# Performance work log

Measured on AMD Instinct MI355X. Metric: run time of the kernel, lower is better.

Reference implementation:

```python
import jax, jax.numpy as jnp
import numpy as np

HEAD_DIM = 64
N_HEADS = 64
N_KV = 8
Q_MULT = N_HEADS // N_KV  # 8
HIDDEN = 2880
SLIDING_WINDOW = 128
BASE = 150000.0
INIT_CTX = 4096
SCALING = 32.0
NTK_ALPHA = 1.0   # beta_slow
NTK_BETA = 32.0   # beta_fast
EPS = 1e-5
SM_SCALE = 1.0 / np.sqrt(HEAD_DIM)


def _cos_sin(num_tokens):
    # YaRN-style NTK rope (scaling_factor > 1 branch)
    freq = BASE ** (jnp.arange(0, HEAD_DIM, 2, dtype=jnp.float32) / HEAD_DIM)
    concentration = 0.1 * np.log(SCALING) + 1.0
    d_half = HEAD_DIM // 2
    low = d_half * np.log(INIT_CTX / (NTK_BETA * 2 * np.pi)) / np.log(BASE)
    high = d_half * np.log(INIT_CTX / (NTK_ALPHA * 2 * np.pi)) / np.log(BASE)
    interpolation = 1.0 / (SCALING * freq)
    extrapolation = 1.0 / freq
    ramp = (jnp.arange(d_half, dtype=jnp.float32) - low) / (high - low)
    mask = 1.0 - jnp.clip(ramp, 0.0, 1.0)
    inv_freq = interpolation * (1.0 - mask) + extrapolation * mask
    t = jnp.arange(num_tokens, dtype=jnp.float32)
    freqs = t[:, None] * inv_freq[None, :]  # [n, d/2]
    return jnp.cos(freqs) * concentration, jnp.sin(freqs) * concentration


def _apply_rotary(x, cos, sin):
    # x: [n, h, d]; cos/sin: [n, d/2]
    cos = cos[:, None, :].astype(x.dtype)
    sin = sin[:, None, :].astype(x.dtype)
    x1, x2 = jnp.split(x, 2, axis=-1)
    return jnp.concatenate((x1 * cos - x2 * sin, x2 * cos + x1 * sin), axis=-1)


def _forward(x, norm_w, qkv_w, out_w, sinks):
    b, s, h = x.shape  # b=1
    n = b * s
    # RMSNorm
    var = jnp.mean(jnp.square(x), axis=-1, keepdims=True)
    t = x * jax.lax.rsqrt(var + EPS) * norm_w
    # QKV projection
    qkv = jnp.einsum('bsh,hf->bsf', t, qkv_w)
    q_dim = N_HEADS * HEAD_DIM
    kv_dim = N_KV * HEAD_DIM
    q = qkv[:, :, :q_dim].reshape(n, N_KV, Q_MULT, HEAD_DIM)
    k = qkv[:, :, q_dim:q_dim + kv_dim].reshape(n, N_KV, HEAD_DIM)
    v = qkv[:, :, q_dim + kv_dim:].reshape(n, N_KV, HEAD_DIM)
    # RoPE
    cos, sin = _cos_sin(n)
    q = _apply_rotary(q.reshape(n, -1, HEAD_DIM), cos, sin).reshape(n, N_KV, Q_MULT, HEAD_DIM)
    k = _apply_rotary(k, cos, sin)
    # sdpa with sliding window + sink logits
    qk = jnp.einsum('qhmd,khd->hmqk', q, k) * SM_SCALE  # [N_KV, Q_MULT, n, n]
    i = jnp.arange(n)[:, None]
    j = jnp.arange(n)[None, :]
    neg_inf = jnp.array(-jnp.inf, dtype=qk.dtype)
    banned = (j > i) | (i - j >= SLIDING_WINDOW)  # causal + sliding window
    qk = jnp.where(banned[None, None, :, :], neg_inf, qk)
    S = jnp.broadcast_to(sinks.reshape(N_KV, Q_MULT, 1, 1), (N_KV, Q_MULT, n, 1))
    logits = jnp.concatenate([qk, S], axis=-1)  # [N_KV, Q_MULT, n, n+1]
    w = jax.nn.softmax(logits, axis=-1)[..., :-1]
    attn = jnp.einsum('hmqk,khd->qhmd', w, v).reshape(n, N_HEADS * HEAD_DIM)
    out = jnp.einsum('qf,fh->qh', attn, out_w)  # [n, hidden]
    return x + out  # broadcasts to [b, s, hidden]


def setup_inputs() -> dict:
    key = jax.random.key(0)
    k1, k2, k3, k4, k5 = jax.random.split(key, 5)
    x = jax.random.normal(k1, (1, 2048, HIDDEN), dtype=jnp.float32)
    norm_w = jax.random.uniform(k2, (HIDDEN,), dtype=jnp.float32, minval=0.5, maxval=1.5)
    qkv_w = jax.random.normal(k3, (HIDDEN, HEAD_DIM * (N_HEADS + 2 * N_KV)), dtype=jnp.float32) * 0.02
    out_w = jax.random.normal(k4, (HEAD_DIM * N_HEADS, HIDDEN), dtype=jnp.float32) * 0.02
    sinks = jax.random.normal(k5, (N_HEADS,), dtype=jnp.float32)
    return {"x": x, "norm_w": norm_w, "qkv_w": qkv_w, "out_w": out_w, "sinks": sinks}


def reference(x, norm_w, qkv_w, out_w, sinks):
    return _forward(x, norm_w, qkv_w, out_w, sinks)
```

## Files before the change

### kernel.cpp

```cpp
#include <hip/hip_runtime.h>
#include <math.h>

typedef unsigned short u16;
typedef unsigned int u32;
typedef short bf4 __attribute__((ext_vector_type(4)));
typedef __bf16 bfv8 __attribute__((ext_vector_type(8)));
typedef float f4 __attribute__((ext_vector_type(4)));

#define SEQ 2048
#define HID 2880
#define KPAD 2944
#define QKVN 5120

static __device__ __forceinline__ u16 f2bf(float x) {
  union { float f; u32 u; } v; v.f = x;
  u32 r = v.u + 0x7fffu + ((v.u >> 16) & 1u);
  return (u16)(r >> 16);
}
static __device__ __forceinline__ float bf2f(u16 s) {
  union { u32 u; float f; } v; v.u = ((u32)s) << 16;
  return v.f;
}
static __device__ __forceinline__ void gl_lds16(const void* g, void* l) {
  __builtin_amdgcn_global_load_lds((const __attribute__((address_space(1))) u32*)g,
                                   (__attribute__((address_space(3))) u32*)l, 16, 0, 0);
}
#define MFMA(a, b, c) __builtin_amdgcn_mfma_f32_16x16x16bf16_1k(a, b, c, 0, 0, 0)
#define MFMA32(a, b, c) __builtin_amdgcn_mfma_f32_16x16x32_bf16(a, b, c, 0, 0, 0)
#define BAR __builtin_amdgcn_s_barrier()
#define SCHEDB __builtin_amdgcn_sched_barrier(0)
#define VMCNT0 asm volatile("s_waitcnt vmcnt(0)" ::: "memory")
#define LGKM0 asm volatile("s_waitcnt lgkmcnt(0)" ::: "memory")
#define LGKM2 asm volatile("s_waitcnt lgkmcnt(2)" ::: "memory")

__global__ __launch_bounds__(256) void k_rmsnorm(const float* __restrict__ x,
                                                 const float* __restrict__ w,
                                                 u16* __restrict__ t) {
  const int row = blockIdx.x;
  const float* xr = x + (size_t)row * HID;
  float ss = 0.f;
  for (int i = threadIdx.x; i < 720; i += 256) {
    float4 v = ((const float4*)xr)[i];
    ss += v.x * v.x + v.y * v.y + v.z * v.z + v.w * v.w;
  }
#pragma unroll
  for (int m = 1; m < 64; m <<= 1) ss += __shfl_xor(ss, m);
  __shared__ float red[4];
  if ((threadIdx.x & 63) == 0) red[threadIdx.x >> 6] = ss;
  __syncthreads();
  float sc = rsqrtf((red[0] + red[1] + red[2] + red[3]) * (1.0f / HID) + 1e-5f);
  u16* tr = t + (size_t)row * KPAD;
  for (int i = threadIdx.x; i < 720; i += 256) {
    float4 v = ((const float4*)xr)[i];
    float4 wv = ((const float4*)w)[i];
    ushort4 o;
    o.x = f2bf(v.x * sc * wv.x);
    o.y = f2bf(v.y * sc * wv.y);
    o.z = f2bf(v.z * sc * wv.z);
    o.w = f2bf(v.w * sc * wv.w);
    ((ushort4*)tr)[i] = o;
  }
  if (threadIdx.x < 16) ((ushort4*)tr)[720 + threadIdx.x] = make_ushort4(0, 0, 0, 0);
}

__global__ __launch_bounds__(256) void k_convT(const float* __restrict__ W,
                                               u16* __restrict__ WT, int K, int Kpad,
                                               int Nsrc) {
  __shared__ u16 tile[64][65];
  const int n0 = blockIdx.x * 64, k0 = blockIdx.y * 64;
  for (int s = threadIdx.x; s < 1024; s += 256) {
    int r = s >> 4, c4 = (s & 15) * 4;
    int kk = k0 + r, nn = n0 + c4;
    float4 v = make_float4(0.f, 0.f, 0.f, 0.f);
    if (kk < K && nn < Nsrc) v = *(const float4*)&W[(size_t)kk * Nsrc + nn];
    tile[c4 + 0][r] = f2bf(v.x);
    tile[c4 + 1][r] = f2bf(v.y);
    tile[c4 + 2][r] = f2bf(v.z);
    tile[c4 + 3][r] = f2bf(v.w);
  }
  __syncthreads();
  for (int s = threadIdx.x; s < 512; s += 256) {
    int r = s >> 3, c8 = (s & 7) * 8;
    u32 p0 = tile[r][c8 + 0] | ((u32)tile[r][c8 + 1] << 16);
    u32 p1 = tile[r][c8 + 2] | ((u32)tile[r][c8 + 3] << 16);
    u32 p2 = tile[r][c8 + 4] | ((u32)tile[r][c8 + 5] << 16);
    u32 p3 = tile[r][c8 + 6] | ((u32)tile[r][c8 + 7] << 16);
    *(uint4*)&WT[(size_t)(n0 + r) * Kpad + k0 + c8] = make_uint4(p0, p1, p2, p3);
  }
}

template <int MODE, int BN>
__global__ __launch_bounds__(256, 2) void k_gemm6(const u16* __restrict__ A,
                                                  const u16* __restrict__ BT,
                                                  void* __restrict__ Cv,
                                                  const float* __restrict__ resid,
                                                  int N, int Nout, int K) {
  constexpr int WN = BN / 2;
  constexpr int NF = WN / 16;
  constexpr int ABY = 128 * 128;
  constexpr int BBY = BN * 128;
  constexpr int TILE = ABY + BBY;
  constexpr int NBC = BBY / 4096;
  __shared__ __align__(16) char lds[2 * TILE];
  const int n0 = blockIdx.x * BN, m0 = blockIdx.y * 128;
  const int tid = threadIdx.x;
  const int l = tid & 63, w = tid >> 6;
  const int wm = w >> 1, wn = w & 1;
  const int g = l >> 4, q = l & 15;
  const int NT = K >> 6;

#define STAGE_A(bo, kt, p) { const int slot = (p)*256 + tid; \
    const int row = slot >> 3, c = slot & 7; \
    gl_lds16(A + (size_t)(m0 + row) * K + (kt)*64 + ((c ^ (row & 7)) * 8), \
             lds + (bo) + slot * 16); }
#define STAGE_B(bo, kt, p) { const int slot = (p)*256 + tid; \
    const int row = slot >> 3, c = slot & 7; \
    gl_lds16(BT + (size_t)(n0 + row) * K + (kt)*64 + ((c ^ (row & 7)) * 8), \
             lds + (bo) + ABY + slot * 16); }
#define LDB2(DST, nf_) { const int r_ = wn * WN + (nf_)*16 + q; \
    DST[0] = *(const bfv8*)(lds + bo + ABY + r_ * 128 + (((g) ^ (r_ & 7)) << 4)); \
    DST[1] = *(const bfv8*)(lds + bo + ABY + r_ * 128 + (((4 + g) ^ (r_ & 7)) << 4)); }

  f4 acc[4][NF] = {};
#pragma unroll
  for (int p = 0; p < 4; ++p) STAGE_A(0, 0, p);
#pragma unroll
  for (int p = 0; p < NBC; ++p) STAGE_B(0, 0, p);
  VMCNT0; SCHEDB; BAR;

  for (int t = 0; t < NT; ++t) {
    const int bo = (t & 1) * TILE;
    const int so = bo ^ TILE;
    if (t + 1 < NT) {
#pragma unroll
      for (int p = 0; p < 4; ++p) STAGE_A(so, t + 1, p);
#pragma unroll
      for (int p = 0; p < NBC; ++p) STAGE_B(so, t + 1, p);
    }
    SCHEDB;
    bfv8 af[4][2], bb[2][2];
#pragma unroll
    for (int mf = 0; mf < 4; ++mf) {
      const int r = wm * 64 + mf * 16 + q;
      af[mf][0] = *(const bfv8*)(lds + bo + r * 128 + (((g) ^ (r & 7)) << 4));
      af[mf][1] = *(const bfv8*)(lds + bo + r * 128 + (((4 + g) ^ (r & 7)) << 4));
    }
    LDB2(bb[0], 0);
    SCHEDB;
    LDB2(bb[1], 1);
    __builtin_amdgcn_s_setprio(1);
#pragma unroll
    for (int nf = 0; nf < NF; ++nf) {
      if (nf == NF - 1) { LGKM0; } else { LGKM2; }
      SCHEDB;
#pragma unroll
      for (int mf = 0; mf < 4; ++mf) {
        acc[mf][nf] = MFMA32(af[mf][0], bb[nf & 1][0], acc[mf][nf]);
        acc[mf][nf] = MFMA32(af[mf][1], bb[nf & 1][1], acc[mf][nf]);
      }
      if (nf + 2 < NF) LDB2(bb[nf & 1], nf + 2);
    }
    __builtin_amdgcn_s_setprio(0);
    VMCNT0;
    SCHEDB; BAR;
  }
#pragma unroll
  for (int mf = 0; mf < 4; ++mf)
#pragma unroll
    for (int nf = 0; nf < NF; ++nf)
#pragma unroll
      for (int r = 0; r < 4; ++r) {
        int row = m0 + wm * 64 + mf * 16 + g * 4 + r;
        int col = n0 + wn * WN + nf * 16 + q;
        if constexpr (MODE == 0) {
          ((u16*)Cv)[(size_t)row * N + col] = f2bf(acc[mf][nf][r]);
        } else {
          if (col < Nout)
            ((float*)Cv)[(size_t)row * Nout + col] =
                acc[mf][nf][r] + resid[(size_t)row * Nout + col];
        }
      }
#undef STAGE_A
#undef STAGE_B
#undef LDB2
}

__global__ __launch_bounds__(256) void k_rope(u16* __restrict__ qkv) {
  __shared__ float lcs[64];
  const int t = blockIdx.x;
  if (threadIdx.x < 32) {
    const int d = threadIdx.x;
    const float low = 8.0927791f, high = 17.3980236f, conc = 1.3465735903f;
    float freq = powf(150000.0f, (float)d * (1.0f / 32.0f));
    float r01 = fminf(fmaxf(((float)d - low) / (high - low), 0.f), 1.f);
    float invf = (1.0f / (32.0f * freq)) * r01 + (1.0f / freq) * (1.f - r01);
    float ang = (float)t * invf;
    lcs[d] = cosf(ang) * conc;
    lcs[d + 32] = sinf(ang) * conc;
  }
  __syncthreads();
  for (int i = threadIdx.x; i < 2304; i += 256) {
    const int d = i & 31, hd = i >> 5;
    u16* base = qkv + (size_t)t * QKVN + (hd < 64 ? hd * 64 : 4096 + (hd - 64) * 64);
    float cc = lcs[d], ss = lcs[d + 32];
    float x1 = bf2f(base[d]), x2 = bf2f(base[d + 32]);
    base[d] = f2bf(x1 * cc - x2 * ss);
    base[d + 32] = f2bf(x2 * cc + x1 * ss);
  }
}

__global__ __launch_bounds__(256) void k_vtrans(const u16* __restrict__ qkv,
                                                u16* __restrict__ vt) {
  __shared__ u16 tile[64][72];
  const int t0 = blockIdx.x * 64, h = blockIdx.y;
  for (int s = threadIdx.x; s < 512; s += 256) {
    int r = s >> 3, c8 = (s & 7) * 8;
    uint4 v = *(const uint4*)&qkv[(size_t)(t0 + r) * QKVN + 4608 + h * 64 + c8];
    *(uint4*)&tile[r][c8] = v;
  }
  __syncthreads();
  for (int s = threadIdx.x; s < 512; s += 256) {
    int d = s >> 3, c8 = (s & 7) * 8;
    u32 p0 = tile[c8 + 0][d] | ((u32)tile[c8 + 1][d] << 16);
    u32 p1 = tile[c8 + 2][d] | ((u32)tile[c8 + 3][d] << 16);
    u32 p2 = tile[c8 + 4][d] | ((u32)tile[c8 + 5][d] << 16);
    u32 p3 = tile[c8 + 6][d] | ((u32)tile[c8 + 7][d] << 16);
    *(uint4*)&vt[((size_t)h * 64 + d) * SEQ + t0 + c8] = make_uint4(p0, p1, p2, p3);
  }
}

__global__ __launch_bounds__(512) void k_attn(const u16* __restrict__ qkv,
                                              const u16* __restrict__ vt,
                                              const float* __restrict__ sinks,
                                              u16* __restrict__ attn) {
  __shared__ u16 lK[144 * 72];
  __shared__ u16 lV[64 * 152];
  __shared__ u16 lP[8 * 16 * 148];
  const int t0 = blockIdx.x * 16;
  const int h = blockIdx.y;
  const int j0 = t0 - 128;
  const int tid = threadIdx.x;
  for (int s = tid; s < 1152; s += 512) {
    int row = s >> 3, c = s & 7;
    int j = j0 + row;
    uint4 v = make_uint4(0, 0, 0, 0);
    if (j >= 0) v = *(const uint4*)&qkv[(size_t)j * QKVN + 4096 + h * 64 + c * 8];
    *(uint4*)&lK[row * 72 + c * 8] = v;
  }
  for (int s = tid; s < 1152; s += 512) {
    int d = s / 18, c = s - d * 18;
    int jb = j0 + c * 8;
    uint4 v = make_uint4(0, 0, 0, 0);
    if (jb >= 0) v = *(const uint4*)&vt[((size_t)h * 64 + d) * SEQ + jb];
    *(uint4*)&lV[d * 152 + c * 8] = v;
  }
  __syncthreads();
  const int w = tid >> 6, l = tid & 63;
  const int g = l >> 4, q = l & 15;
  const int hq = h * 8 + w;
  const float sink = sinks[hq];
  bf4 qf[4];
  const u16* qrow = qkv + (size_t)(t0 + q) * QKVN + hq * 64;
#pragma unroll
  for (int ks = 0; ks < 4; ++ks) qf[ks] = *(const bf4*)&qrow[ks * 16 + g * 4];
  f4 sacc[9];
#pragma unroll
  for (int nt = 0; nt < 9; ++nt) {
    f4 z = {0.f, 0.f, 0.f, 0.f};
    sacc[nt] = z;
#pragma unroll
    for (int ks = 0; ks < 4; ++ks) {
      bf4 kf = *(const bf4*)&lK[(nt * 16 + q) * 72 + ks * 16 + g * 4];
      sacc[nt] = MFMA(qf[ks], kf, sacc[nt]);
    }
  }
  const float NEG = -__builtin_inff();
  float rmax[4] = {NEG, NEG, NEG, NEG};
#pragma unroll
  for (int nt = 0; nt < 9; ++nt)
#pragma unroll
    for (int r = 0; r < 4; ++r) {
      float sv = sacc[nt][r] * 0.125f;
      int it = t0 + g * 4 + r;
      int j = j0 + nt * 16 + q;
      bool ban = (j > it) || (it - j >= 128) || (j < 0);
      sv = ban ? NEG : sv;
      sacc[nt][r] = sv;
      rmax[r] = fmaxf(rmax[r], sv);
    }
#pragma unroll
  for (int r = 0; r < 4; ++r)
#pragma unroll
    for (int m = 1; m < 16; m <<= 1) rmax[r] = fmaxf(rmax[r], __shfl_xor(rmax[r], m));
  float ssum[4];
  u16* pbase = lP + w * (16 * 148);
#pragma unroll
  for (int r = 0; r < 4; ++r) {
    float mf = fmaxf(rmax[r], sink);
    float ps = 0.f;
#pragma unroll
    for (int nt = 0; nt < 9; ++nt) {
      float p = __expf(sacc[nt][r] - mf);
      pbase[(g * 4 + r) * 148 + nt * 16 + q] = f2bf(p);
      ps += p;
    }
#pragma unroll
    for (int m = 1; m < 16; m <<= 1) ps += __shfl_xor(ps, m);
    ssum[r] = ps + __expf(sink - mf);
  }
  f4 oacc[4] = {};
#pragma unroll
  for (int kt = 0; kt < 9; ++kt) {
    bf4 pa = *(const bf4*)&pbase[q * 148 + kt * 16 + g * 4];
#pragma unroll
    for (int nt = 0; nt < 4; ++nt) {
      bf4 vf = *(const bf4*)&lV[(nt * 16 + q) * 152 + kt * 16 + g * 4];
      oacc[nt] = MFMA(pa, vf, oacc[nt]);
    }
  }
#pragma unroll
  for (int nt = 0; nt < 4; ++nt)
#pragma unroll
    for (int r = 0; r < 4; ++r) {
      int row = t0 + g * 4 + r;
      attn[(size_t)row * 4096 + hq * 64 + nt * 16 + q] = f2bf(oacc[nt][r] / ssum[r]);
    }
}

extern "C" void kernel_launch(void* const* d_in, const int* in_sizes, int n_in,
                              void* d_out, int out_size, void* d_ws, size_t ws_size,
                              hipStream_t stream) {
  const float* x = (const float*)d_in[0];
  const float* norm_w = (const float*)d_in[1];
  const float* qkv_w = (const float*)d_in[2];
  const float* out_w = (const float*)d_in[3];
  const float* sinks = (const float*)d_in[4];
  float* out = (float*)d_out;
  char* ws = (char*)d_ws;
  u16* t     = (u16*)(ws);
  u16* wqkvT = (u16*)(ws + 12058624);
  u16* qkv   = (u16*)(ws + 42205184);
  u16* vt    = (u16*)(ws + 63176704);
  u16* woutT = (u16*)(ws + 65273856);
  u16* attnO = (u16*)(ws);

  k_rmsnorm<<<dim3(2048), dim3(256), 0, stream>>>(x, norm_w, t);
  k_convT<<<dim3(80, 46), dim3(256), 0, stream>>>(qkv_w, wqkvT, 2880, KPAD, 5120);
  k_convT<<<dim3(48, 64), dim3(256), 0, stream>>>(out_w, woutT, 4096, 4096, 2880);
  k_gemm6<0, 160><<<dim3(32, 16), dim3(256), 0, stream>>>(t, wqkvT, (void*)qkv,
                                                          nullptr, 5120, 5120, KPAD);
  k_rope<<<dim3(2048), dim3(256), 0, stream>>>(qkv);
  k_vtrans<<<dim3(32, 8), dim3(256), 0, stream>>>(qkv, vt);
  k_attn<<<dim3(128, 8), dim3(512), 0, stream>>>(qkv, vt, sinks, attnO);
  k_gemm6<1, 96><<<dim3(32, 16), dim3(256), 0, stream>>>(attnO, woutT, (void*)out,
                                                         x, 3072, 2880, 4096);
}
```

Measured before the change: 175.4 us.

## Restructure GEMM main loop with per-wave staging and cross-iteration fragment prefetch

The bf16 MFMA GEMM used for both the QKV and output projections is rewritten. Each wave now stages only the A/B tile rows it consumes first, and the next tile's own A fragments and first B chunk are preloaded from LDS before the last MFMA group of the current tile. The loop is unrolled by two with ping-pong fragment registers and fine-grained lgkmcnt waits, and B chunk order is rotated per wave row to spread LDS bank access. The aim is to hide LDS-read and global-load latency behind MFMAs. The cost is more live registers and a design that assumes NF is 3 or 5 and NT is even.

```diff
diff --git a/kernel.cpp b/kernel.cpp
--- a/kernel.cpp
+++ b/kernel.cpp
@@ -30,8 +30,7 @@
 #define BAR __builtin_amdgcn_s_barrier()
 #define SCHEDB __builtin_amdgcn_sched_barrier(0)
 #define VMCNT0 asm volatile("s_waitcnt vmcnt(0)" ::: "memory")
-#define LGKM0 asm volatile("s_waitcnt lgkmcnt(0)" ::: "memory")
-#define LGKM2 asm volatile("s_waitcnt lgkmcnt(2)" ::: "memory")
+#define LGKMN(n) asm volatile("s_waitcnt lgkmcnt(" #n ")" ::: "memory")
 
 __global__ __launch_bounds__(256) void k_rmsnorm(const float* __restrict__ x,
                                                  const float* __restrict__ w,
@@ -90,17 +89,17 @@
 }
 
 template <int MODE, int BN>
-__global__ __launch_bounds__(256, 2) void k_gemm6(const u16* __restrict__ A,
+__global__ __launch_bounds__(256, 2) void k_gemm7(const u16* __restrict__ A,
                                                   const u16* __restrict__ BT,
                                                   void* __restrict__ Cv,
                                                   const float* __restrict__ resid,
                                                   int N, int Nout, int K) {
   constexpr int WN = BN / 2;
   constexpr int NF = WN / 16;
+  constexpr int CK1 = (NF + 1) / 2;
   constexpr int ABY = 128 * 128;
   constexpr int BBY = BN * 128;
   constexpr int TILE = ABY + BBY;
-  constexpr int NBC = BBY / 4096;
   __shared__ __align__(16) char lds[2 * TILE];
   const int n0 = blockIdx.x * BN, m0 = blockIdx.y * 128;
   const int tid = threadIdx.x;
@@ -108,81 +107,111 @@
   const int wm = w >> 1, wn = w & 1;
   const int g = l >> 4, q = l & 15;
   const int NT = K >> 6;
-
-#define STAGE_A(bo, kt, p) { const int slot = (p)*256 + tid; \
-    const int row = slot >> 3, c = slot & 7; \
-    gl_lds16(A + (size_t)(m0 + row) * K + (kt)*64 + ((c ^ (row & 7)) * 8), \
-             lds + (bo) + slot * 16); }
-#define STAGE_B(bo, kt, p) { const int slot = (p)*256 + tid; \
-    const int row = slot >> 3, c = slot & 7; \
-    gl_lds16(BT + (size_t)(n0 + row) * K + (kt)*64 + ((c ^ (row & 7)) * 8), \
-             lds + (bo) + ABY + slot * 16); }
-#define LDB2(DST, nf_) { const int r_ = wn * WN + (nf_)*16 + q; \
-    DST[0] = *(const bfv8*)(lds + bo + ABY + r_ * 128 + (((g) ^ (r_ & 7)) << 4)); \
-    DST[1] = *(const bfv8*)(lds + bo + ABY + r_ * 128 + (((4 + g) ^ (r_ & 7)) << 4)); }
+  const int rowSb = wm * 64 + wn * 32;
+  const int rowOb = wm * 64 + 32 - wn * 32;
+  const int bQ = wm ? CK1 * 16 : 0;
+  const int nBc = (wm ? (NF - CK1) : CK1) * 2;
+  int ck[NF];
+#pragma unroll
+  for (int p = 0; p < NF; ++p) {
+    int c = p + (wm ? CK1 : 0);
+    ck[p] = (c >= NF) ? c - NF : c;
+  }
+
+#define STAGE_A7(so_, kt) { _Pragma("unroll") for (int p = 0; p < 4; ++p) { \
+    const int row = rowSb + p * 8 + (l >> 3); \
+    gl_lds16(A + (size_t)(m0 + row) * K + (kt) * 64 + (((l & 7) ^ (row & 7)) * 8), \
+             lds + (so_) + (rowSb + p * 8) * 128 + l * 16); } }
+#define STAGE_B7(so_, kt) { _Pragma("unroll") for (int p = 0; p < 2 * CK1; ++p) if (p < nBc) { \
+    const int rb = wn * WN + bQ + p * 8; \
+    const int row = rb + (l >> 3); \
+    gl_lds16(BT + (size_t)(n0 + row) * K + (kt) * 64 + (((l & 7) ^ (row & 7)) * 8), \
+             lds + (so_) + ABY + rb * 128 + l * 16); } }
+#define LDF2(DST, rb, bo_) { const int r_ = (rb) + q; \
+    DST[0] = *(const bfv8*)(lds + (bo_) + r_ * 128 + (((g) ^ (r_ & 7)) << 4)); \
+    DST[1] = *(const bfv8*)(lds + (bo_) + r_ * 128 + (((4 + g) ^ (r_ & 7)) << 4)); }
+#define LDBC(DST, chunk, bo_) { const int r_ = wn * WN + (chunk) * 16 + q; \
+    DST[0] = *(const bfv8*)(lds + (bo_) + ABY + r_ * 128 + (((g) ^ (r_ & 7)) << 4)); \
+    DST[1] = *(const bfv8*)(lds + (bo_) + ABY + r_ * 128 + (((4 + g) ^ (r_ & 7)) << 4)); }
+#define MM2(ac, AF, BB) { ac = MFMA32(AF[0], BB[0], ac); ac = MFMA32(AF[1], BB[1], ac); }
+#define MM8(pos, BB, AFS) { MM2(acc[0][pos], AFS[0], BB); MM2(acc[1][pos], AFS[1], BB); \
+                            MM2(acc[2][pos], afO[0], BB); MM2(acc[3][pos], afO[1], BB); }
+
+#define TB7(t_, S, AFS_C, AFS_N) { \
+    const int t__ = (t_); const bool pf__ = (t__ + 1 < NT); \
+    const int bo = (t__ & 1) * TILE, so = bo ^ TILE; \
+    LDF2(afO[0], rowOb, bo); LDF2(afO[1], rowOb + 16, bo);   \
+    LDBC(bb[(S) ^ 1], ck[1], bo); \
+    SCHEDB; \
+    if (pf__) { STAGE_A7(so, t__ + 1); STAGE_B7(so, t__ + 1); } \
+    SCHEDB; \
+    __builtin_amdgcn_s_setprio(1); \
+    LGKMN(6); SCHEDB;   \
+    MM2(acc[0][0], AFS_C[0], bb[S]); MM2(acc[1][0], AFS_C[1], bb[S]); \
+    LGKMN(2); SCHEDB;   \
+    MM2(acc[2][0], afO[0], bb[S]); MM2(acc[3][0], afO[1], bb[S]); \
+    LDBC(bb[S], ck[2], bo); \
+    LGKMN(2); SCHEDB;   \
+    MM8(1, bb[(S) ^ 1], AFS_C); \
+    if constexpr (NF == 5) { \
+      LDBC(bb[(S) ^ 1], ck[3], bo); \
+      LGKMN(2); SCHEDB; \
+      MM8(2, bb[S], AFS_C); \
+      LDBC(bb[S], ck[4], bo); \
+      LGKMN(2); SCHEDB; \
+      MM8(3, bb[(S) ^ 1], AFS_C); \
+    } \
+    if (pf__) { \
+      VMCNT0; SCHEDB;   \
+      LDF2(AFS_N[0], rowSb, so); LDF2(AFS_N[1], rowSb + 16, so); \
+      LDBC(bb[(S) ^ 1], ck[0], so); \
+      LGKMN(6); \
+    } else { LGKMN(0); } \
+    SCHEDB; \
+    MM8(NF - 1, bb[S], AFS_C); \
+    __builtin_amdgcn_s_setprio(0); \
+    SCHEDB; BAR; \
+  }
 
   f4 acc[4][NF] = {};
-#pragma unroll
-  for (int p = 0; p < 4; ++p) STAGE_A(0, 0, p);
-#pragma unroll
-  for (int p = 0; p < NBC; ++p) STAGE_B(0, 0, p);
-  VMCNT0; SCHEDB; BAR;
-
-  for (int t = 0; t < NT; ++t) {
-    const int bo = (t & 1) * TILE;
-    const int so = bo ^ TILE;
-    if (t + 1 < NT) {
-#pragma unroll
-      for (int p = 0; p < 4; ++p) STAGE_A(so, t + 1, p);
-#pragma unroll
-      for (int p = 0; p < NBC; ++p) STAGE_B(so, t + 1, p);
-    }
-    SCHEDB;
-    bfv8 af[4][2], bb[2][2];
-#pragma unroll
-    for (int mf = 0; mf < 4; ++mf) {
-      const int r = wm * 64 + mf * 16 + q;
-      af[mf][0] = *(const bfv8*)(lds + bo + r * 128 + (((g) ^ (r & 7)) << 4));
-      af[mf][1] = *(const bfv8*)(lds + bo + r * 128 + (((4 + g) ^ (r & 7)) << 4));
-    }
-    LDB2(bb[0], 0);
-    SCHEDB;
-    LDB2(bb[1], 1);
-    __builtin_amdgcn_s_setprio(1);
-#pragma unroll
-    for (int nf = 0; nf < NF; ++nf) {
-      if (nf == NF - 1) { LGKM0; } else { LGKM2; }
-      SCHEDB;
-#pragma unroll
-      for (int mf = 0; mf < 4; ++mf) {
-        acc[mf][nf] = MFMA32(af[mf][0], bb[nf & 1][0], acc[mf][nf]);
-        acc[mf][nf] = MFMA32(af[mf][1], bb[nf & 1][1], acc[mf][nf]);
-      }
-      if (nf + 2 < NF) LDB2(bb[nf & 1], nf + 2);
-    }
-    __builtin_amdgcn_s_setprio(0);
-    VMCNT0;
-    SCHEDB; BAR;
-  }
-#pragma unroll
-  for (int mf = 0; mf < 4; ++mf)
-#pragma unroll
-    for (int nf = 0; nf < NF; ++nf)
+  bfv8 afSP[2][2], afSQ[2][2], afO[2][2], bb[2][2];
+
+  STAGE_A7(0, 0); STAGE_B7(0, 0);
+  VMCNT0; SCHEDB;
+  LDF2(afSP[0], rowSb, 0); LDF2(afSP[1], rowSb + 16, 0);
+  LDBC(bb[0], ck[0], 0);
+  SCHEDB; BAR;
+
+  for (int t = 0; t < NT; t += 2) {
+    TB7(t, 0, afSP, afSQ);
+    TB7(t + 1, 1, afSQ, afSP);
+  }
+#pragma unroll
+  for (int mf = 0; mf < 4; ++mf) {
+    const int rb = (mf < 2) ? (rowSb + mf * 16) : (rowOb + (mf - 2) * 16);
+#pragma unroll
+    for (int pos = 0; pos < NF; ++pos) {
+      const int col = n0 + wn * WN + ck[pos] * 16 + q;
 #pragma unroll
       for (int r = 0; r < 4; ++r) {
-        int row = m0 + wm * 64 + mf * 16 + g * 4 + r;
-        int col = n0 + wn * WN + nf * 16 + q;
+        int row = m0 + rb + g * 4 + r;
         if constexpr (MODE == 0) {
-          ((u16*)Cv)[(size_t)row * N + col] = f2bf(acc[mf][nf][r]);
+          ((u16*)Cv)[(size_t)row * N + col] = f2bf(acc[mf][pos][r]);
         } else {
           if (col < Nout)
             ((float*)Cv)[(size_t)row * Nout + col] =
-                acc[mf][nf][r] + resid[(size_t)row * Nout + col];
+                acc[mf][pos][r] + resid[(size_t)row * Nout + col];
         }
       }
-#undef STAGE_A
-#undef STAGE_B
-#undef LDB2
+    }
+  }
+#undef STAGE_A7
+#undef STAGE_B7
+#undef LDF2
+#undef LDBC
+#undef MM2
+#undef MM8
+#undef TB7
 }
 
 __global__ __launch_bounds__(256) void k_rope(u16* __restrict__ qkv) {
@@ -347,11 +376,11 @@
   k_rmsnorm<<<dim3(2048), dim3(256), 0, stream>>>(x, norm_w, t);
   k_convT<<<dim3(80, 46), dim3(256), 0, stream>>>(qkv_w, wqkvT, 2880, KPAD, 5120);
   k_convT<<<dim3(48, 64), dim3(256), 0, stream>>>(out_w, woutT, 4096, 4096, 2880);
-  k_gemm6<0, 160><<<dim3(32, 16), dim3(256), 0, stream>>>(t, wqkvT, (void*)qkv,
+  k_gemm7<0, 160><<<dim3(32, 16), dim3(256), 0, stream>>>(t, wqkvT, (void*)qkv,
                                                           nullptr, 5120, 5120, KPAD);
   k_rope<<<dim3(2048), dim3(256), 0, stream>>>(qkv);
   k_vtrans<<<dim3(32, 8), dim3(256), 0, stream>>>(qkv, vt);
   k_attn<<<dim3(128, 8), dim3(512), 0, stream>>>(qkv, vt, sinks, attnO);
-  k_gemm6<1, 96><<<dim3(32, 16), dim3(256), 0, stream>>>(attnO, woutT, (void*)out,
+  k_gemm7<1, 96><<<dim3(32, 16), dim3(256), 0, stream>>>(attnO, woutT, (void*)out,
                                                          x, 3072, 2880, 4096);
 }
```

Result: slower. 184.4 us (+5.1%).

## Load GEMM A operand straight to registers and swizzle blocks across XCDs

Applied to the files above, without the earlier changes.

The GEMM kernel stops staging the A tile through LDS. Each wave now loads its A fragments directly from global memory into double-buffered registers, prefetching one k-step ahead, and the k-loop is unrolled by two so the two register buffers swap roles. The 2D grid becomes a 1D launch remapped so that blocks on the same XCD share N-columns, aiming for better L2 reuse. This shrinks LDS use and removes the LDS round trip for A, but the two waves that share A rows now each fetch them, and the global loads are only partly coalesced, which adds cache traffic and load latency.

```diff
diff --git a/kernel.cpp b/kernel.cpp
--- a/kernel.cpp
+++ b/kernel.cpp
@@ -90,79 +90,72 @@
 }
 
 template <int MODE, int BN>
-__global__ __launch_bounds__(256, 2) void k_gemm6(const u16* __restrict__ A,
+__global__ __launch_bounds__(256, 2) void k_gemm8(const u16* __restrict__ A,
                                                   const u16* __restrict__ BT,
                                                   void* __restrict__ Cv,
                                                   const float* __restrict__ resid,
                                                   int N, int Nout, int K) {
   constexpr int WN = BN / 2;
   constexpr int NF = WN / 16;
-  constexpr int ABY = 128 * 128;
-  constexpr int BBY = BN * 128;
-  constexpr int TILE = ABY + BBY;
-  constexpr int NBC = BBY / 4096;
+  constexpr int TILE = BN * 128;
+  constexpr int NBC = TILE / 4096;
   __shared__ __align__(16) char lds[2 * TILE];
-  const int n0 = blockIdx.x * BN, m0 = blockIdx.y * 128;
+  const int bid = blockIdx.x;
+  const int xcd = bid & 7, idx = bid >> 3;
+  const int n0 = (xcd * 4 + (idx >> 4)) * BN;
+  const int m0 = (idx & 15) * 128;
   const int tid = threadIdx.x;
   const int l = tid & 63, w = tid >> 6;
   const int wm = w >> 1, wn = w & 1;
   const int g = l >> 4, q = l & 15;
   const int NT = K >> 6;
-
-#define STAGE_A(bo, kt, p) { const int slot = (p)*256 + tid; \
-    const int row = slot >> 3, c = slot & 7; \
-    gl_lds16(A + (size_t)(m0 + row) * K + (kt)*64 + ((c ^ (row & 7)) * 8), \
-             lds + (bo) + slot * 16); }
-#define STAGE_B(bo, kt, p) { const int slot = (p)*256 + tid; \
+  const u16* aBase = A + (size_t)(m0 + wm * 64 + q) * K + g * 8;
+
+#define STAGE_B8(bo_, kt) { _Pragma("unroll") for (int p = 0; p < NBC; ++p) { \
+    const int slot = p * 256 + tid; \
     const int row = slot >> 3, c = slot & 7; \
     gl_lds16(BT + (size_t)(n0 + row) * K + (kt)*64 + ((c ^ (row & 7)) * 8), \
-             lds + (bo) + ABY + slot * 16); }
-#define LDB2(DST, nf_) { const int r_ = wn * WN + (nf_)*16 + q; \
-    DST[0] = *(const bfv8*)(lds + bo + ABY + r_ * 128 + (((g) ^ (r_ & 7)) << 4)); \
-    DST[1] = *(const bfv8*)(lds + bo + ABY + r_ * 128 + (((4 + g) ^ (r_ & 7)) << 4)); }
+             lds + (bo_) + slot * 16); } }
+#define ALOAD(DST, kt) { _Pragma("unroll") for (int mf = 0; mf < 4; ++mf) { \
+    DST[mf][0] = *(const bfv8*)(aBase + (size_t)(mf * 16) * K + (kt)*64); \
+    DST[mf][1] = *(const bfv8*)(aBase + (size_t)(mf * 16) * K + (kt)*64 + 32); } }
+#define LDB2(DST, nf_, bo_) { const int r_ = wn * WN + (nf_)*16 + q; \
+    DST[0] = *(const bfv8*)(lds + (bo_) + r_ * 128 + (((g) ^ (r_ & 7)) << 4)); \
+    DST[1] = *(const bfv8*)(lds + (bo_) + r_ * 128 + (((4 + g) ^ (r_ & 7)) << 4)); }
+
+#define TB8(t_, ACUR, ANXT) { \
+    const int t__ = (t_); const bool pf__ = (t__ + 1 < NT); \
+    const int bo = (t__ & 1) * TILE, so = bo ^ TILE; \
+    if (pf__) { STAGE_B8(so, t__ + 1); ALOAD(ANXT, t__ + 1); } \
+    SCHEDB; \
+    LDB2(bb[0], 0, bo); \
+    SCHEDB; \
+    LDB2(bb[1], 1, bo); \
+    __builtin_amdgcn_s_setprio(1); \
+    _Pragma("unroll") for (int nf = 0; nf < NF; ++nf) { \
+      if (nf == NF - 1) { LGKM0; } else { LGKM2; } \
+      SCHEDB; \
+      _Pragma("unroll") for (int mf = 0; mf < 4; ++mf) { \
+        acc[mf][nf] = MFMA32(ACUR[mf][0], bb[nf & 1][0], acc[mf][nf]); \
+        acc[mf][nf] = MFMA32(ACUR[mf][1], bb[nf & 1][1], acc[mf][nf]); \
+      } \
+      if (nf + 2 < NF) LDB2(bb[nf & 1], nf + 2, bo); \
+    } \
+    __builtin_amdgcn_s_setprio(0); \
+    VMCNT0;   \
+    SCHEDB; BAR; \
+  }
 
   f4 acc[4][NF] = {};
-#pragma unroll
-  for (int p = 0; p < 4; ++p) STAGE_A(0, 0, p);
-#pragma unroll
-  for (int p = 0; p < NBC; ++p) STAGE_B(0, 0, p);
+  bfv8 aP[4][2], aQ[4][2], bb[2][2];
+
+  STAGE_B8(0, 0);
+  ALOAD(aP, 0);
   VMCNT0; SCHEDB; BAR;
 
-  for (int t = 0; t < NT; ++t) {
-    const int bo = (t & 1) * TILE;
-    const int so = bo ^ TILE;
-    if (t + 1 < NT) {
-#pragma unroll
-      for (int p = 0; p < 4; ++p) STAGE_A(so, t + 1, p);
-#pragma unroll
-      for (int p = 0; p < NBC; ++p) STAGE_B(so, t + 1, p);
-    }
-    SCHEDB;
-    bfv8 af[4][2], bb[2][2];
-#pragma unroll
-    for (int mf = 0; mf < 4; ++mf) {
-      const int r = wm * 64 + mf * 16 + q;
-      af[mf][0] = *(const bfv8*)(lds + bo + r * 128 + (((g) ^ (r & 7)) << 4));
-      af[mf][1] = *(const bfv8*)(lds + bo + r * 128 + (((4 + g) ^ (r & 7)) << 4));
-    }
-    LDB2(bb[0], 0);
-    SCHEDB;
-    LDB2(bb[1], 1);
-    __builtin_amdgcn_s_setprio(1);
-#pragma unroll
-    for (int nf = 0; nf < NF; ++nf) {
-      if (nf == NF - 1) { LGKM0; } else { LGKM2; }
-      SCHEDB;
-#pragma unroll
-      for (int mf = 0; mf < 4; ++mf) {
-        acc[mf][nf] = MFMA32(af[mf][0], bb[nf & 1][0], acc[mf][nf]);
-        acc[mf][nf] = MFMA32(af[mf][1], bb[nf & 1][1], acc[mf][nf]);
-      }
-      if (nf + 2 < NF) LDB2(bb[nf & 1], nf + 2);
-    }
-    __builtin_amdgcn_s_setprio(0);
-    VMCNT0;
-    SCHEDB; BAR;
+  for (int t = 0; t < NT; t += 2) {
+    TB8(t, aP, aQ);
+    TB8(t + 1, aQ, aP);
   }
 #pragma unroll
   for (int mf = 0; mf < 4; ++mf)
@@ -180,9 +173,10 @@
                 acc[mf][nf][r] + resid[(size_t)row * Nout + col];
         }
       }
-#undef STAGE_A
-#undef STAGE_B
+#undef STAGE_B8
+#undef ALOAD
 #undef LDB2
+#undef TB8
 }
 
 __global__ __launch_bounds__(256) void k_rope(u16* __restrict__ qkv) {
@@ -347,11 +341,11 @@
   k_rmsnorm<<<dim3(2048), dim3(256), 0, stream>>>(x, norm_w, t);
   k_convT<<<dim3(80, 46), dim3(256), 0, stream>>>(qkv_w, wqkvT, 2880, KPAD, 5120);
   k_convT<<<dim3(48, 64), dim3(256), 0, stream>>>(out_w, woutT, 4096, 4096, 2880);
-  k_gemm6<0, 160><<<dim3(32, 16), dim3(256), 0, stream>>>(t, wqkvT, (void*)qkv,
-                                                          nullptr, 5120, 5120, KPAD);
+  k_gemm8<0, 160><<<dim3(512), dim3(256), 0, stream>>>(t, wqkvT, (void*)qkv,
+                                                       nullptr, 5120, 5120, KPAD);
   k_rope<<<dim3(2048), dim3(256), 0, stream>>>(qkv);
   k_vtrans<<<dim3(32, 8), dim3(256), 0, stream>>>(qkv, vt);
   k_attn<<<dim3(128, 8), dim3(512), 0, stream>>>(qkv, vt, sinks, attnO);
-  k_gemm6<1, 96><<<dim3(32, 16), dim3(256), 0, stream>>>(attnO, woutT, (void*)out,
-                                                         x, 3072, 2880, 4096);
-}
+  k_gemm8<1, 96><<<dim3(512), dim3(256), 0, stream>>>(attnO, woutT, (void*)out,
+                                                      x, 3072, 2880, 4096);
+}
```

New measurement: 318.8 us. 81.8% more time.

## Fuse RoPE into attention kernel using precomputed cos/sin table

Applied to the files above, without the earlier changes.

Removes the standalone RoPE kernel, which did a read-modify-write pass over q and k in the qkv buffer. The cos/sin table is now computed per row inside the RMSNorm kernel and stored in workspace. The attention kernel rotates K in LDS after staging and rotates its Q fragments in registers. K rows are now rotated redundantly by each of the 128 query blocks per head, which adds compute and an extra barrier inside attention.

```diff
diff --git a/kernel.cpp b/kernel.cpp
--- a/kernel.cpp
+++ b/kernel.cpp
@@ -35,8 +35,19 @@
 
 __global__ __launch_bounds__(256) void k_rmsnorm(const float* __restrict__ x,
                                                  const float* __restrict__ w,
-                                                 u16* __restrict__ t) {
+                                                 u16* __restrict__ t,
+                                                 float* __restrict__ tab) {
   const int row = blockIdx.x;
+  if (threadIdx.x < 32) {
+    const int d = threadIdx.x;
+    const float low = 8.0927791f, high = 17.3980236f, conc = 1.3465735903f;
+    float freq = powf(150000.0f, (float)d * (1.0f / 32.0f));
+    float r01 = fminf(fmaxf(((float)d - low) / (high - low), 0.f), 1.f);
+    float invf = (1.0f / (32.0f * freq)) * r01 + (1.0f / freq) * (1.f - r01);
+    float ang = (float)row * invf;
+    tab[(size_t)row * 64 + d] = cosf(ang) * conc;
+    tab[(size_t)row * 64 + 32 + d] = sinf(ang) * conc;
+  }
   const float* xr = x + (size_t)row * HID;
   float ss = 0.f;
   for (int i = threadIdx.x; i < 720; i += 256) {
@@ -109,14 +120,14 @@
   const int g = l >> 4, q = l & 15;
   const int NT = K >> 6;
 
-#define STAGE_A(bo, kt, p) { const int slot = (p)*256 + tid; \
+#define STAGE_A(bo_, kt, p) { const int slot = (p)*256 + tid; \
     const int row = slot >> 3, c = slot & 7; \
     gl_lds16(A + (size_t)(m0 + row) * K + (kt)*64 + ((c ^ (row & 7)) * 8), \
-             lds + (bo) + slot * 16); }
-#define STAGE_B(bo, kt, p) { const int slot = (p)*256 + tid; \
+             lds + (bo_) + slot * 16); }
+#define STAGE_B(bo_, kt, p) { const int slot = (p)*256 + tid; \
     const int row = slot >> 3, c = slot & 7; \
     gl_lds16(BT + (size_t)(n0 + row) * K + (kt)*64 + ((c ^ (row & 7)) * 8), \
-             lds + (bo) + ABY + slot * 16); }
+             lds + (bo_) + ABY + slot * 16); }
 #define LDB2(DST, nf_) { const int r_ = wn * WN + (nf_)*16 + q; \
     DST[0] = *(const bfv8*)(lds + bo + ABY + r_ * 128 + (((g) ^ (r_ & 7)) << 4)); \
     DST[1] = *(const bfv8*)(lds + bo + ABY + r_ * 128 + (((4 + g) ^ (r_ & 7)) << 4)); }
@@ -185,30 +196,6 @@
 #undef LDB2
 }
 
-__global__ __launch_bounds__(256) void k_rope(u16* __restrict__ qkv) {
-  __shared__ float lcs[64];
-  const int t = blockIdx.x;
-  if (threadIdx.x < 32) {
-    const int d = threadIdx.x;
-    const float low = 8.0927791f, high = 17.3980236f, conc = 1.3465735903f;
-    float freq = powf(150000.0f, (float)d * (1.0f / 32.0f));
-    float r01 = fminf(fmaxf(((float)d - low) / (high - low), 0.f), 1.f);
-    float invf = (1.0f / (32.0f * freq)) * r01 + (1.0f / freq) * (1.f - r01);
-    float ang = (float)t * invf;
-    lcs[d] = cosf(ang) * conc;
-    lcs[d + 32] = sinf(ang) * conc;
-  }
-  __syncthreads();
-  for (int i = threadIdx.x; i < 2304; i += 256) {
-    const int d = i & 31, hd = i >> 5;
-    u16* base = qkv + (size_t)t * QKVN + (hd < 64 ? hd * 64 : 4096 + (hd - 64) * 64);
-    float cc = lcs[d], ss = lcs[d + 32];
-    float x1 = bf2f(base[d]), x2 = bf2f(base[d + 32]);
-    base[d] = f2bf(x1 * cc - x2 * ss);
-    base[d + 32] = f2bf(x2 * cc + x1 * ss);
-  }
-}
-
 __global__ __launch_bounds__(256) void k_vtrans(const u16* __restrict__ qkv,
                                                 u16* __restrict__ vt) {
   __shared__ u16 tile[64][72];
@@ -232,6 +219,7 @@
 __global__ __launch_bounds__(512) void k_attn(const u16* __restrict__ qkv,
                                               const u16* __restrict__ vt,
                                               const float* __restrict__ sinks,
+                                              const float* __restrict__ tab,
                                               u16* __restrict__ attn) {
   __shared__ u16 lK[144 * 72];
   __shared__ u16 lV[64 * 152];
@@ -255,6 +243,19 @@
     *(uint4*)&lV[d * 152 + c * 8] = v;
   }
   __syncthreads();
+  for (int p = tid; p < 4608; p += 512) {
+    int row = p >> 5, d = p & 31;
+    int j = j0 + row;
+    if (j >= 0) {
+      float c = tab[(size_t)j * 64 + d];
+      float s = tab[(size_t)j * 64 + 32 + d];
+      int base = row * 72;
+      float x1 = bf2f(lK[base + d]), x2 = bf2f(lK[base + 32 + d]);
+      lK[base + d] = f2bf(x1 * c - x2 * s);
+      lK[base + 32 + d] = f2bf(x2 * c + x1 * s);
+    }
+  }
+  __syncthreads();
   const int w = tid >> 6, l = tid & 63;
   const int g = l >> 4, q = l & 15;
   const int hq = h * 8 + w;
@@ -263,6 +264,23 @@
   const u16* qrow = qkv + (size_t)(t0 + q) * QKVN + hq * 64;
 #pragma unroll
   for (int ks = 0; ks < 4; ++ks) qf[ks] = *(const bf4*)&qrow[ks * 16 + g * 4];
+  {
+    const float* tb = tab + (size_t)(t0 + q) * 64;
+    float c0[4], s0[4], c1[4], s1[4];
+    *(float4*)c0 = *(const float4*)&tb[g * 4];
+    *(float4*)s0 = *(const float4*)&tb[32 + g * 4];
+    *(float4*)c1 = *(const float4*)&tb[16 + g * 4];
+    *(float4*)s1 = *(const float4*)&tb[48 + g * 4];
+#pragma unroll
+    for (int i = 0; i < 4; ++i) {
+      float x0 = bf2f((u16)qf[0][i]), x2 = bf2f((u16)qf[2][i]);
+      qf[0][i] = (short)f2bf(x0 * c0[i] - x2 * s0[i]);
+      qf[2][i] = (short)f2bf(x2 * c0[i] + x0 * s0[i]);
+      float x1 = bf2f((u16)qf[1][i]), x3 = bf2f((u16)qf[3][i]);
+      qf[1][i] = (short)f2bf(x1 * c1[i] - x3 * s1[i]);
+      qf[3][i] = (short)f2bf(x3 * c1[i] + x1 * s1[i]);
+    }
+  }
   f4 sacc[9];
 #pragma unroll
   for (int nt = 0; nt < 9; ++nt) {
@@ -342,16 +360,16 @@
   u16* qkv   = (u16*)(ws + 42205184);
   u16* vt    = (u16*)(ws + 63176704);
   u16* woutT = (u16*)(ws + 65273856);
+  float* tab = (float*)(ws + 90439680);
   u16* attnO = (u16*)(ws);
 
-  k_rmsnorm<<<dim3(2048), dim3(256), 0, stream>>>(x, norm_w, t);
+  k_rmsnorm<<<dim3(2048), dim3(256), 0, stream>>>(x, norm_w, t, tab);
   k_convT<<<dim3(80, 46), dim3(256), 0, stream>>>(qkv_w, wqkvT, 2880, KPAD, 5120);
   k_convT<<<dim3(48, 64), dim3(256), 0, stream>>>(out_w, woutT, 4096, 4096, 2880);
   k_gemm6<0, 160><<<dim3(32, 16), dim3(256), 0, stream>>>(t, wqkvT, (void*)qkv,
                                                           nullptr, 5120, 5120, KPAD);
-  k_rope<<<dim3(2048), dim3(256), 0, stream>>>(qkv);
   k_vtrans<<<dim3(32, 8), dim3(256), 0, stream>>>(qkv, vt);
-  k_attn<<<dim3(128, 8), dim3(512), 0, stream>>>(qkv, vt, sinks, attnO);
+  k_attn<<<dim3(128, 8), dim3(512), 0, stream>>>(qkv, vt, sinks, tab, attnO);
   k_gemm6<1, 96><<<dim3(32, 16), dim3(256), 0, stream>>>(attnO, woutT, (void*)out,
                                                          x, 3072, 2880, 4096);
 }
```

Result: no change. 177.0 us (+0.9%).
